# Optimization experiments

Hardware: AMD Instinct MI355X
Metric: run time of the kernel (lower is better)

The kernel has to match this reference:

```python
import jax, jax.numpy as jnp
import numpy as np

K = 10  # kNN neighbors (module default)


def _safe_norm(x):
    # norm along last axis with zero (not NaN) gradient at x == 0
    sq = jnp.sum(x * x, axis=-1)
    safe = jnp.where(sq > 0, sq, 1.0)
    return jnp.where(sq > 0, jnp.sqrt(safe), 0.0)


def _angle(v1, v2):
    cross = jnp.cross(v1, v2, axis=-1)
    dot = jnp.sum(v1 * v2, axis=-1)
    return jnp.arctan2(_safe_norm(cross), dot)


def _compute_normals(p, k):
    # squared pairwise distances (same kNN ordering as cdist, cheaper/safer)
    sq = jnp.sum((p[:, None, :] - p[None, :, :]) ** 2, axis=-1)  # (N,N)
    _, knn = jax.lax.top_k(-sq, k + 1)
    knn = knn[:, 1:]                        # drop self, (N,k)
    neigh = p[knn]                          # (N,k,3)
    centered = neigh - neigh.mean(axis=1, keepdims=True)
    cov = jnp.einsum('nki,nkj->nij', centered, centered) / k  # (N,3,3)
    _, eigvecs = jnp.linalg.eigh(cov)
    return eigvecs[:, :, 0]                 # smallest-eigenvalue eigenvector, (N,3)


def reference(points, W, b):
    p = points[0]                           # (N,3)
    n = _compute_normals(p, K)              # (N,3)
    d = p[:, None, :] - p[None, :, :]       # (N,N,3), d[i,j] = p_i - p_j
    ni = jnp.broadcast_to(n[:, None, :], d.shape)
    nj = jnp.broadcast_to(n[None, :, :], d.shape)
    ppf = jnp.stack([
        _safe_norm(d),
        _angle(ni, d),
        _angle(nj, d),
        _angle(ni, nj),
    ], axis=-1)                             # (N,N,4)
    feat = ppf.mean(axis=1)                 # (N,4)
    s = feat @ W.T + b                      # (N,out)
    return s[None]                          # (1,N,out)


def setup_inputs() -> dict:
    key = jax.random.key(0)
    k1, k2 = jax.random.split(key)
    N, OUT = 2048, 256
    points = jax.random.normal(k1, (1, N, 3), dtype=jnp.float32)
    W = jax.random.normal(k2, (OUT, 4), dtype=jnp.float32) * 0.1
    b = jnp.zeros((OUT,), dtype=jnp.float32)
    return {"points": points, "W": W, "b": b}
```

## Files before the change

kernel.cpp:

```cpp
#include <hip/hip_runtime.h>
#include <math.h>

#pragma clang fp contract(off)

#define NPTS 2048
#define KNN 10
#define NOUT 256


__device__ __forceinline__ float lapy2f(float x, float y) {
  float xa = fabsf(x), ya = fabsf(y);
  float w = fmaxf(xa, ya), z = fminf(xa, ya);
  if (z == 0.f) return w;
  float t = z / w;
  return w * sqrtf(1.f + t * t);
}

__device__ __forceinline__ void slartgf(float f, float g, float& c, float& s, float& r) {
  if (g == 0.f) { c = 1.f; s = 0.f; r = f; }
  else if (f == 0.f) { c = 0.f; s = copysignf(1.f, g); r = fabsf(g); }
  else {
    float d = sqrtf(f * f + g * g);
    float p = 1.f / d;
    c = fabsf(f) * p;
    s = g * copysignf(p, f);
    r = copysignf(d, f);
  }
}

__device__ __forceinline__ void slaev2f(float a, float b, float c,
                                        float& rt1, float& rt2, float& cs1, float& sn1) {
  float sm = a + c;
  float df = a - c;
  float adf = fabsf(df);
  float tb = b + b;
  float ab = fabsf(tb);
  float acmx, acmn;
  if (fabsf(a) > fabsf(c)) { acmx = a; acmn = c; } else { acmx = c; acmn = a; }
  float rt;
  if (adf > ab)      { float t = ab / adf; rt = adf * sqrtf(1.f + t * t); }
  else if (adf < ab) { float t = adf / ab; rt = ab * sqrtf(1.f + t * t); }
  else               { rt = ab * sqrtf(2.f); }
  int sgn1;
  if (sm < 0.f) {
    rt1 = 0.5f * (sm - rt); sgn1 = -1;
    rt2 = (acmx / rt1) * acmn - (b / rt1) * b;
  } else if (sm > 0.f) {
    rt1 = 0.5f * (sm + rt); sgn1 = 1;
    rt2 = (acmx / rt1) * acmn - (b / rt1) * b;
  } else {
    rt1 = 0.5f * rt; rt2 = -0.5f * rt; sgn1 = 1;
  }
  int sgn2; float cs;
  if (df >= 0.f) { cs = df + rt; sgn2 = 1; } else { cs = df - rt; sgn2 = -1; }
  float acs = fabsf(cs);
  if (acs > ab) {
    float ct = -tb / cs;
    sn1 = 1.f / sqrtf(1.f + ct * ct);
    cs1 = ct * sn1;
  } else {
    if (ab == 0.f) { cs1 = 1.f; sn1 = 0.f; }
    else {
      float tn = -cs / tb;
      cs1 = 1.f / sqrtf(1.f + tn * tn);
      sn1 = tn * cs1;
    }
  }
  if (sgn1 == sgn2) { float tn = cs1; cs1 = -sn1; sn1 = tn; }
}

#define ROT12(c, s) {                                         \
    float t_;                                                 \
    t_ = z01; z01 = (c) * t_ - (s) * z00; z00 = (s) * t_ + (c) * z00; \
    t_ = z11; z11 = (c) * t_ - (s) * z10; z10 = (s) * t_ + (c) * z10; \
    t_ = z21; z21 = (c) * t_ - (s) * z20; z20 = (s) * t_ + (c) * z20; }
#define ROT23(c, s) {                                         \
    float t_;                                                 \
    t_ = z02; z02 = (c) * t_ - (s) * z01; z01 = (s) * t_ + (c) * z01; \
    t_ = z12; z12 = (c) * t_ - (s) * z11; z11 = (s) * t_ + (c) * z11; \
    t_ = z22; z22 = (c) * t_ - (s) * z21; z21 = (s) * t_ + (c) * z21; }

__device__ __forceinline__ void ssteqr3_reg(
    float& d0, float& d1, float& d2, float& e0, float& e1,
    float& z00, float& z01, float& z02,
    float& z10, float& z11, float& z12,
    float& z20, float& z21, float& z22) {
  const float eps = 5.9604645e-8f;
  const float eps2 = eps * eps;
  const float safmin = 1.1754944e-38f;
  const int nmaxit = 90;
  int jtot = 0;
  int l1 = 1;
  for (int og = 0; og < 4; ++og) {
    if (l1 > 3) break;
    if (l1 == 2) e0 = 0.f;
    else if (l1 == 3) e1 = 0.f;
    int m = 3;
    if (l1 == 1) {
      float t = fabsf(e0);
      if (t == 0.f) m = 1;
      else if (t <= (sqrtf(fabsf(d0)) * sqrtf(fabsf(d1))) * eps) { e0 = 0.f; m = 1; }
      else {
        float t2 = fabsf(e1);
        if (t2 == 0.f) m = 2;
        else if (t2 <= (sqrtf(fabsf(d1)) * sqrtf(fabsf(d2))) * eps) { e1 = 0.f; m = 2; }
      }
    } else if (l1 == 2) {
      float t = fabsf(e1);
      if (t == 0.f) m = 2;
      else if (t <= (sqrtf(fabsf(d1)) * sqrtf(fabsf(d2))) * eps) { e1 = 0.f; m = 2; }
    }
    int l = l1, lend = m;
    l1 = m + 1;
    if (lend == l) continue;
    {
      float dlend = (lend == 1) ? d0 : ((lend == 2) ? d1 : d2);
      float dl = (l == 1) ? d0 : ((l == 2) ? d1 : d2);
      if (fabsf(dlend) < fabsf(dl)) { int t = lend; lend = l; l = t; }
    }
    if (lend > l) {
      for (int it = 0; it < 128; ++it) {
        int m2 = lend;
        if (l != lend) {
          for (int mm = l; mm <= lend - 1; ++mm) {
            float em  = (mm == 1) ? e0 : e1;
            float dm1 = (mm == 1) ? d0 : d1;
            float dm  = (mm == 1) ? d1 : d2;
            float tst = em * em;
            if (tst <= (eps2 * fabsf(dm1)) * fabsf(dm) + safmin) { m2 = mm; break; }
          }
        }
        if (m2 < lend) { if (m2 == 1) e0 = 0.f; else e1 = 0.f; }
        float p = (l == 1) ? d0 : ((l == 2) ? d1 : d2);
        if (m2 == l) { l += 1; if (l <= lend) continue; break; }
        if (m2 == l + 1) {
          float rt1, rt2, c, s;
          if (l == 1) {
            slaev2f(d0, e0, d1, rt1, rt2, c, s);
            ROT12(c, s)
            d0 = rt1; d1 = rt2; e0 = 0.f;
          } else {
            slaev2f(d1, e1, d2, rt1, rt2, c, s);
            ROT23(c, s)
            d1 = rt1; d2 = rt2; e1 = 0.f;
          }
          l += 2; if (l <= lend) continue; break;
        }
        if (jtot == nmaxit) break;
        jtot++;
        float g = (d1 - p) / (2.f * e0);
        float r = lapy2f(g, 1.f);
        g = d2 - p + e0 / (g + copysignf(r, g));
        float s = 1.f, c = 1.f;
        p = 0.f;
        float c0, s0n, c1, s1n;
        {
          float f = s * e1;
          float bb = c * e1;
          slartgf(g, f, c, s, r);
          g = d2 - p;
          r = (d1 - g) * s + 2.f * c * bb;
          p = s * r;
          d2 = g + p;
          g = c * r - bb;
          c1 = c; s1n = -s;
        }
        {
          float f = s * e0;
          float bb = c * e0;
          slartgf(g, f, c, s, r);
          e1 = r;
          g = d1 - p;
          r = (d0 - g) * s + 2.f * c * bb;
          p = s * r;
          d1 = g + p;
          g = c * r - bb;
          c0 = c; s0n = -s;
        }
        ROT23(c1, s1n)
        ROT12(c0, s0n)
        d0 = d0 - p;
        e0 = g;
      }
    } else {
      for (int it = 0; it < 128; ++it) {
        int m2 = lend;
        if (l != lend) {
          for (int mm = l; mm >= lend + 1; --mm) {
            float em  = (mm == 3) ? e1 : e0;
            float dm1 = (mm == 3) ? d2 : d1;
            float dm2 = (mm == 3) ? d1 : d0;
            float tst = em * em;
            if (tst <= (eps2 * fabsf(dm1)) * fabsf(dm2) + safmin) { m2 = mm; break; }
          }
        }
        if (m2 > lend) { if (m2 == 3) e1 = 0.f; else e0 = 0.f; }
        float p = (l == 1) ? d0 : ((l == 2) ? d1 : d2);
        if (m2 == l) { l -= 1; if (l >= lend) continue; break; }
        if (m2 == l - 1) {
          float rt1, rt2, c, s;
          if (l == 2) {
            slaev2f(d0, e0, d1, rt1, rt2, c, s);
            ROT12(c, s)
            d0 = rt1; d1 = rt2; e0 = 0.f;
          } else {
            slaev2f(d1, e1, d2, rt1, rt2, c, s);
            ROT23(c, s)
            d1 = rt1; d2 = rt2; e1 = 0.f;
          }
          l -= 2; if (l >= lend) continue; break;
        }
        if (jtot == nmaxit) break;
        jtot++;
        float g = (d1 - p) / (2.f * e1);
        float r = lapy2f(g, 1.f);
        g = d0 - p + e1 / (g + copysignf(r, g));
        float s = 1.f, c = 1.f;
        p = 0.f;
        float c0, s0p, c1, s1p;
        {
          float f = s * e0;
          float bb = c * e0;
          slartgf(g, f, c, s, r);
          g = d0 - p;
          r = (d1 - g) * s + 2.f * c * bb;
          p = s * r;
          d0 = g + p;
          g = c * r - bb;
          c0 = c; s0p = s;
        }
        {
          float f = s * e1;
          float bb = c * e1;
          slartgf(g, f, c, s, r);
          e0 = r;
          g = d1 - p;
          r = (d2 - g) * s + 2.f * c * bb;
          p = s * r;
          d1 = g + p;
          g = c * r - bb;
          c1 = c; s1p = s;
        }
        ROT12(c0, s0p)
        ROT23(c1, s1p)
        d2 = d2 - p;
        e1 = g;
      }
    }
  }
  {
    int k = 1; float p = d0;
    if (d1 < p) { k = 2; p = d1; }
    if (d2 < p) { k = 3; p = d2; }
    if (k == 2) {
      d1 = d0; d0 = p;
      float t;
      t = z00; z00 = z01; z01 = t;
      t = z10; z10 = z11; z11 = t;
      t = z20; z20 = z21; z21 = t;
    } else if (k == 3) {
      d2 = d0; d0 = p;
      float t;
      t = z00; z00 = z02; z02 = t;
      t = z10; z10 = z12; z12 = t;
      t = z20; z20 = z22; z22 = t;
    }
    k = 2; p = d1;
    if (d2 < p) { k = 3; p = d2; }
    if (k == 3) {
      d2 = d1; d1 = p;
      float t;
      t = z01; z01 = z02; z02 = t;
      t = z11; z11 = z12; z12 = t;
      t = z21; z21 = z22; z22 = t;
    }
  }
}


__global__ __launch_bounds__(256) void knn_normals_kernel(
    const float* __restrict__ pts,
    float* __restrict__ pxa, float* __restrict__ pya, float* __restrict__ pza,
    float* __restrict__ nxa, float* __restrict__ nya, float* __restrict__ nza) {
  __shared__ int knn_lds[4][KNN];
  const int tid = threadIdx.x;
  const int lane = tid & 63;
  const int wv = tid >> 6;

  {
    const int p = 4 * blockIdx.x + wv;
    float px = pts[3 * p], py = pts[3 * p + 1], pz = pts[3 * p + 2];
    if (lane == 0) { pxa[p] = px; pya[p] = py; pza[p] = pz; }

    unsigned long long k0[8], k1[8], k2[8], k3[8];
#define DIST(g, arr)                                                      \
    {                                                                     \
      _Pragma("unroll")                                                   \
      for (int t = 0; t < 8; ++t) {                                       \
        int j = ((g) * 8 + t) * 64 + lane;                                \
        float dx = px - pts[3 * j];                                       \
        float dy = py - pts[3 * j + 1];                                   \
        float dz = pz - pts[3 * j + 2];                                   \
        float sq = dx * dx;                                               \
        sq = sq + dy * dy;                                                \
        sq = sq + dz * dz;                                                \
        arr[t] = (((unsigned long long)__float_as_uint(sq)) << 32) |      \
                 (unsigned int)j;                                         \
      }                                                                   \
    }
    DIST(0, k0) DIST(1, k1) DIST(2, k2) DIST(3, k3)
#undef DIST

#define CE(arr, a, b)                                                     \
    {                                                                     \
      unsigned long long lo = arr[a] < arr[b] ? arr[a] : arr[b];          \
      unsigned long long hi = arr[a] < arr[b] ? arr[b] : arr[a];          \
      arr[a] = lo; arr[b] = hi;                                           \
    }
#define SORT8(arr)                                                        \
    CE(arr, 0, 1) CE(arr, 2, 3) CE(arr, 4, 5) CE(arr, 6, 7)               \
    CE(arr, 0, 2) CE(arr, 1, 3) CE(arr, 4, 6) CE(arr, 5, 7)               \
    CE(arr, 1, 2) CE(arr, 5, 6) CE(arr, 0, 4) CE(arr, 3, 7)               \
    CE(arr, 1, 5) CE(arr, 2, 6)                                           \
    CE(arr, 1, 4) CE(arr, 3, 6)                                           \
    CE(arr, 2, 4) CE(arr, 3, 5)                                           \
    CE(arr, 3, 4)
    SORT8(k0) SORT8(k1) SORT8(k2) SORT8(k3)
#undef SORT8
#undef CE

#define POP(arr)                                                          \
    {                                                                     \
      _Pragma("unroll")                                                   \
      for (int q = 0; q < 7; ++q) arr[q] = arr[q + 1];                    \
      arr[7] = 0xFFFFFFFFFFFFFFFFULL;                                     \
    }
    for (int r = 0; r < KNN + 1; ++r) {
      unsigned long long h01 = k0[0] < k1[0] ? k0[0] : k1[0];
      unsigned long long h23 = k2[0] < k3[0] ? k2[0] : k3[0];
      unsigned long long h = h01 < h23 ? h01 : h23;
      unsigned long long m = h;
#pragma unroll
      for (int off = 32; off > 0; off >>= 1) {
        unsigned long long o = __shfl_xor(m, off, 64);
        m = (o < m) ? o : m;
      }
      if (r > 0 && lane == 0) knn_lds[wv][r - 1] = (int)(unsigned int)m;
      if (h == m) {
        if (k0[0] == m)      { POP(k0) }
        else if (k1[0] == m) { POP(k1) }
        else if (k2[0] == m) { POP(k2) }
        else                 { POP(k3) }
      }
    }
#undef POP
  }
  __syncthreads();

  if (tid < 4) {
    const int p = 4 * blockIdx.x + tid;
    float nx[KNN], ny[KNN], nz[KNN];
    float sx = 0.f, sy = 0.f, sz = 0.f;
#pragma unroll
    for (int t = 0; t < KNN; ++t) {
      int j = knn_lds[tid][t];
      nx[t] = pts[3 * j]; ny[t] = pts[3 * j + 1]; nz[t] = pts[3 * j + 2];
      sx = sx + nx[t]; sy = sy + ny[t]; sz = sz + nz[t];
    }
    float mx = sx / 10.f, my = sy / 10.f, mz = sz / 10.f;
    float a11 = 0.f, a21 = 0.f, a31 = 0.f, a22 = 0.f, a32 = 0.f, a33 = 0.f;
#pragma unroll
    for (int t = 0; t < KNN; ++t) {
      float cx = nx[t] - mx, cy = ny[t] - my, cz = nz[t] - mz;
      a11 = a11 + cx * cx;
      a21 = a21 + cy * cx;
      a31 = a31 + cz * cx;
      a22 = a22 + cy * cy;
      a32 = a32 + cz * cy;
      a33 = a33 + cz * cz;
    }
    a11 = a11 / 10.f; a21 = a21 / 10.f; a31 = a31 / 10.f;
    a22 = a22 / 10.f; a32 = a32 / 10.f; a33 = a33 / 10.f;

    float d0, d1, d2, e0, e1, tau1 = 0.f, v2 = 0.f;
    {
      float alpha = a21;
      float xnorm = fabsf(a31);
      if (xnorm == 0.f) {
        tau1 = 0.f; v2 = 0.f;
        d0 = a11; d1 = a22; d2 = a33; e0 = alpha; e1 = a32;
      } else {
        float beta = -copysignf(lapy2f(alpha, xnorm), alpha);
        tau1 = (beta - alpha) / beta;
        v2 = a31 * (1.f / (alpha - beta));
        float y1 = tau1 * a22; y1 = y1 + tau1 * (a32 * v2);
        float y2 = tau1 * a32; y2 = y2 + (tau1 * v2) * a33;
        float dotv = y1; dotv = dotv + y2 * v2;
        float ac = -0.5f * tau1 * dotv;
        y1 = y1 + ac;
        y2 = y2 + ac * v2;
        float t1 = -y1, t2 = -1.f;
        a22 = (a22 + t1) + y1 * t2;
        a32 = (a32 + v2 * t1) + y2 * t2;
        float t1b = -y2, t2b = -v2;
        a33 = (a33 + v2 * t1b) + y2 * t2b;
        d0 = a11; d1 = a22; d2 = a33; e0 = beta; e1 = a32;
      }
    }
    float z00 = 1.f, z01 = 0.f, z02 = 0.f;
    float z10 = 0.f, z11 = 1.f, z12 = 0.f;
    float z20 = 0.f, z21 = 0.f, z22 = 1.f;
    ssteqr3_reg(d0, d1, d2, e0, e1,
                z00, z01, z02, z10, z11, z12, z20, z21, z22);
    if (tau1 != 0.f) {
      float w = tau1 * (z10 + v2 * z20);
      z10 = z10 - w;
      z20 = z20 - v2 * w;
    }
    nxa[p] = z00;
    nya[p] = z10;
    nza[p] = z20;
  }
}


__device__ __forceinline__ float atan2_pos(float y, float x) {
#pragma clang fp contract(fast)
  float axx = fabsf(x);
  float mn = fminf(axx, y), mx = fmaxf(axx, y);
  float a = mn * __builtin_amdgcn_rcpf(mx);
  a = (mx == 0.f) ? 0.f : a;
  float s = a * a;
  float r = a * (0.9998660f +
           s * (-0.3302995f +
           s * (0.1801410f +
           s * (-0.0851330f +
           s * 0.0208351f))));
  r = (y > axx) ? 1.57079632679f - r : r;
  r = (x < 0.f) ? 3.14159265359f - r : r;
  return r;
}

__device__ __forceinline__ float angle3(float ax, float ay, float az,
                                        float bx, float by, float bz) {
#pragma clang fp contract(fast)
  float cx = ay * bz - az * by;
  float cy = az * bx - ax * bz;
  float cz = ax * by - ay * bx;
  float sq = cx * cx + cy * cy + cz * cz;
  float dot = ax * bx + ay * by + az * bz;
  return atan2_pos(sqrtf(sq), dot);
}

__global__ __launch_bounds__(256) void ppf_kernel(
    const float* __restrict__ pxa, const float* __restrict__ pya,
    const float* __restrict__ pza, const float* __restrict__ nxa,
    const float* __restrict__ nya, const float* __restrict__ nza,
    const float* __restrict__ Wm, const float* __restrict__ bias,
    float* __restrict__ out) {
#pragma clang fp contract(fast)
  const int tid = threadIdx.x;
  const int lane = tid & 63;
  const int wv = tid >> 6;
  const int i = 4 * blockIdx.x + wv;

  float pxi = pxa[i], pyi = pya[i], pzi = pza[i];
  float ax = nxa[i], ay = nya[i], az = nza[i];

  float s0 = 0.f, s1 = 0.f, s2 = 0.f, s3 = 0.f;
#pragma unroll 4
  for (int it = 0; it < NPTS / 64; ++it) {
    int j = it * 64 + lane;
    float dx = pxi - pxa[j];
    float dy = pyi - pya[j];
    float dz = pzi - pza[j];
    float bx = nxa[j], by = nya[j], bz = nza[j];
    float sq = dx * dx + dy * dy + dz * dz;
    s0 += sqrtf(sq);
    s1 += angle3(ax, ay, az, dx, dy, dz);
    s2 += angle3(bx, by, bz, dx, dy, dz);
    s3 += angle3(ax, ay, az, bx, by, bz);
  }

#pragma unroll
  for (int off = 1; off < 64; off <<= 1) {
    s0 += __shfl_xor(s0, off, 64);
    s1 += __shfl_xor(s1, off, 64);
    s2 += __shfl_xor(s2, off, 64);
    s3 += __shfl_xor(s3, off, 64);
  }
  const float inv = 1.f / 2048.f;
  float f0 = s0 * inv, f1 = s1 * inv, f2 = s2 * inv, f3 = s3 * inv;

  const float4* W4 = (const float4*)Wm;
  const float4* b4 = (const float4*)bias;
  float4 bb = b4[lane];
  float4 w0 = W4[4 * lane + 0];
  float4 w1 = W4[4 * lane + 1];
  float4 w2 = W4[4 * lane + 2];
  float4 w3 = W4[4 * lane + 3];
  float4 r;
  r.x = (((f0 * w0.x + f1 * w0.y) + f2 * w0.z) + f3 * w0.w) + bb.x;
  r.y = (((f0 * w1.x + f1 * w1.y) + f2 * w1.z) + f3 * w1.w) + bb.y;
  r.z = (((f0 * w2.x + f1 * w2.y) + f2 * w2.z) + f3 * w2.w) + bb.z;
  r.w = (((f0 * w3.x + f1 * w3.y) + f2 * w3.z) + f3 * w3.w) + bb.w;
  ((float4*)(out + (size_t)i * NOUT))[lane] = r;
}


extern "C" void kernel_launch(void* const* d_in, const int* in_sizes, int n_in,
                              void* d_out, int out_size, void* d_ws, size_t ws_size,
                              hipStream_t stream) {
  const float* pts = (const float*)d_in[0];
  const float* Wm  = (const float*)d_in[1];
  const float* bs  = (const float*)d_in[2];
  float* out = (float*)d_out;

  float* pxa = (float*)d_ws;
  float* pya = pxa + NPTS;
  float* pza = pya + NPTS;
  float* nxa = pza + NPTS;
  float* nya = nxa + NPTS;
  float* nza = nya + NPTS;

  knn_normals_kernel<<<NPTS / 4, 256, 0, stream>>>(pts, pxa, pya, pza, nxa, nya, nza);
  ppf_kernel<<<NPTS / 4, 256, 0, stream>>>(pxa, pya, pza, nxa, nya, nza, Wm, bs, out);
}
```

Before: 110.3 us.

## Split each point across four wavefronts in kNN and PPF kernels

Both kernels now give one point to a whole 256-thread block instead of one point per wavefront. Each wave handles a quarter of the candidates and combines its partial top-11 or partial sums through shared memory; the kNN merge ranks the 44 candidates. The aim is four times more blocks, more parallelism across the GPU and shorter serial loops per wave. In exchange it adds block synchronisation and a single-thread normal computation in every block. It also switches sqrt to the raw AMDGPU builtin.

Measured after the change: 99.44 us. -9.9%, faster.

```diff
diff --git a/kernel.cpp b/kernel.cpp
--- a/kernel.cpp
+++ b/kernel.cpp
@@ -282,88 +282,79 @@
     const float* __restrict__ pts,
     float* __restrict__ pxa, float* __restrict__ pya, float* __restrict__ pza,
     float* __restrict__ nxa, float* __restrict__ nya, float* __restrict__ nza) {
-  __shared__ int knn_lds[4][KNN];
+  __shared__ unsigned long long cand[4 * (KNN + 1)];
+  __shared__ int knn_sh[KNN];
   const int tid = threadIdx.x;
   const int lane = tid & 63;
   const int wv = tid >> 6;
+  const int p = blockIdx.x;
 
   {
-    const int p = 4 * blockIdx.x + wv;
     float px = pts[3 * p], py = pts[3 * p + 1], pz = pts[3 * p + 2];
-    if (lane == 0) { pxa[p] = px; pya[p] = py; pza[p] = pz; }
-
-    unsigned long long k0[8], k1[8], k2[8], k3[8];
-#define DIST(g, arr)                                                      \
+    if (tid == 0) { pxa[p] = px; pya[p] = py; pza[p] = pz; }
+
+    unsigned long long k0[8];
+#pragma unroll
+    for (int t = 0; t < 8; ++t) {
+      int j = wv * 512 + t * 64 + lane;
+      float dx = px - pts[3 * j];
+      float dy = py - pts[3 * j + 1];
+      float dz = pz - pts[3 * j + 2];
+      float sq = dx * dx;
+      sq = sq + dy * dy;
+      sq = sq + dz * dz;
+      k0[t] = (((unsigned long long)__float_as_uint(sq)) << 32) |
+              (unsigned int)j;
+    }
+
+#define CE(a, b)                                                          \
     {                                                                     \
-      _Pragma("unroll")                                                   \
-      for (int t = 0; t < 8; ++t) {                                       \
-        int j = ((g) * 8 + t) * 64 + lane;                                \
-        float dx = px - pts[3 * j];                                       \
-        float dy = py - pts[3 * j + 1];                                   \
-        float dz = pz - pts[3 * j + 2];                                   \
-        float sq = dx * dx;                                               \
-        sq = sq + dy * dy;                                                \
-        sq = sq + dz * dz;                                                \
-        arr[t] = (((unsigned long long)__float_as_uint(sq)) << 32) |      \
-                 (unsigned int)j;                                         \
-      }                                                                   \
-    }
-    DIST(0, k0) DIST(1, k1) DIST(2, k2) DIST(3, k3)
-#undef DIST
-
-#define CE(arr, a, b)                                                     \
-    {                                                                     \
-      unsigned long long lo = arr[a] < arr[b] ? arr[a] : arr[b];          \
-      unsigned long long hi = arr[a] < arr[b] ? arr[b] : arr[a];          \
-      arr[a] = lo; arr[b] = hi;                                           \
-    }
-#define SORT8(arr)                                                        \
-    CE(arr, 0, 1) CE(arr, 2, 3) CE(arr, 4, 5) CE(arr, 6, 7)               \
-    CE(arr, 0, 2) CE(arr, 1, 3) CE(arr, 4, 6) CE(arr, 5, 7)               \
-    CE(arr, 1, 2) CE(arr, 5, 6) CE(arr, 0, 4) CE(arr, 3, 7)               \
-    CE(arr, 1, 5) CE(arr, 2, 6)                                           \
-    CE(arr, 1, 4) CE(arr, 3, 6)                                           \
-    CE(arr, 2, 4) CE(arr, 3, 5)                                           \
-    CE(arr, 3, 4)
-    SORT8(k0) SORT8(k1) SORT8(k2) SORT8(k3)
-#undef SORT8
+      unsigned long long lo = k0[a] < k0[b] ? k0[a] : k0[b];              \
+      unsigned long long hi = k0[a] < k0[b] ? k0[b] : k0[a];              \
+      k0[a] = lo; k0[b] = hi;                                             \
+    }
+    CE(0, 1) CE(2, 3) CE(4, 5) CE(6, 7)
+    CE(0, 2) CE(1, 3) CE(4, 6) CE(5, 7)
+    CE(1, 2) CE(5, 6) CE(0, 4) CE(3, 7)
+    CE(1, 5) CE(2, 6)
+    CE(1, 4) CE(3, 6)
+    CE(2, 4) CE(3, 5)
+    CE(3, 4)
 #undef CE
 
-#define POP(arr)                                                          \
-    {                                                                     \
-      _Pragma("unroll")                                                   \
-      for (int q = 0; q < 7; ++q) arr[q] = arr[q + 1];                    \
-      arr[7] = 0xFFFFFFFFFFFFFFFFULL;                                     \
-    }
     for (int r = 0; r < KNN + 1; ++r) {
-      unsigned long long h01 = k0[0] < k1[0] ? k0[0] : k1[0];
-      unsigned long long h23 = k2[0] < k3[0] ? k2[0] : k3[0];
-      unsigned long long h = h01 < h23 ? h01 : h23;
-      unsigned long long m = h;
+      unsigned long long m = k0[0];
 #pragma unroll
       for (int off = 32; off > 0; off >>= 1) {
         unsigned long long o = __shfl_xor(m, off, 64);
         m = (o < m) ? o : m;
       }
-      if (r > 0 && lane == 0) knn_lds[wv][r - 1] = (int)(unsigned int)m;
-      if (h == m) {
-        if (k0[0] == m)      { POP(k0) }
-        else if (k1[0] == m) { POP(k1) }
-        else if (k2[0] == m) { POP(k2) }
-        else                 { POP(k3) }
+      if (lane == 0) cand[wv * (KNN + 1) + r] = m;
+      if (k0[0] == m) {
+#pragma unroll
+        for (int q = 0; q < 7; ++q) k0[q] = k0[q + 1];
+        k0[7] = 0xFFFFFFFFFFFFFFFFULL;
       }
     }
-#undef POP
   }
   __syncthreads();
 
-  if (tid < 4) {
-    const int p = 4 * blockIdx.x + tid;
+  if (tid < 4 * (KNN + 1)) {
+    unsigned long long e = cand[tid];
+    int rank = 0;
+#pragma unroll
+    for (int m = 0; m < 4 * (KNN + 1); ++m) rank += (cand[m] < e) ? 1 : 0;
+    if (rank > 0 && rank <= KNN)
+      knn_sh[rank - 1] = (int)(unsigned int)(e & 0xFFFFFFFFULL);
+  }
+  __syncthreads();
+
+  if (tid == 0) {
     float nx[KNN], ny[KNN], nz[KNN];
     float sx = 0.f, sy = 0.f, sz = 0.f;
 #pragma unroll
     for (int t = 0; t < KNN; ++t) {
-      int j = knn_lds[tid][t];
+      int j = knn_sh[t];
       nx[t] = pts[3 * j]; ny[t] = pts[3 * j + 1]; nz[t] = pts[3 * j + 2];
       sx = sx + nx[t]; sy = sy + ny[t]; sz = sz + nz[t];
     }
@@ -449,7 +440,7 @@
   float cz = ax * by - ay * bx;
   float sq = cx * cx + cy * cy + cz * cz;
   float dot = ax * bx + ay * by + az * bz;
-  return atan2_pos(sqrtf(sq), dot);
+  return atan2_pos(__builtin_amdgcn_sqrtf(sq), dot);
 }
 
 __global__ __launch_bounds__(256) void ppf_kernel(
@@ -459,24 +450,25 @@
     const float* __restrict__ Wm, const float* __restrict__ bias,
     float* __restrict__ out) {
 #pragma clang fp contract(fast)
+  __shared__ float ps[4][4];
   const int tid = threadIdx.x;
   const int lane = tid & 63;
   const int wv = tid >> 6;
-  const int i = 4 * blockIdx.x + wv;
+  const int i = blockIdx.x;
 
   float pxi = pxa[i], pyi = pya[i], pzi = pza[i];
   float ax = nxa[i], ay = nya[i], az = nza[i];
 
   float s0 = 0.f, s1 = 0.f, s2 = 0.f, s3 = 0.f;
-#pragma unroll 4
-  for (int it = 0; it < NPTS / 64; ++it) {
-    int j = it * 64 + lane;
+#pragma unroll
+  for (int it = 0; it < 8; ++it) {
+    int j = wv * 512 + it * 64 + lane;
     float dx = pxi - pxa[j];
     float dy = pyi - pya[j];
     float dz = pzi - pza[j];
     float bx = nxa[j], by = nya[j], bz = nza[j];
     float sq = dx * dx + dy * dy + dz * dz;
-    s0 += sqrtf(sq);
+    s0 += __builtin_amdgcn_sqrtf(sq);
     s1 += angle3(ax, ay, az, dx, dy, dz);
     s2 += angle3(bx, by, bz, dx, dy, dz);
     s3 += angle3(ax, ay, az, bx, by, bz);
@@ -489,22 +481,18 @@
     s2 += __shfl_xor(s2, off, 64);
     s3 += __shfl_xor(s3, off, 64);
   }
+  if (lane == 0) { ps[wv][0] = s0; ps[wv][1] = s1; ps[wv][2] = s2; ps[wv][3] = s3; }
+  __syncthreads();
+
   const float inv = 1.f / 2048.f;
-  float f0 = s0 * inv, f1 = s1 * inv, f2 = s2 * inv, f3 = s3 * inv;
-
-  const float4* W4 = (const float4*)Wm;
-  const float4* b4 = (const float4*)bias;
-  float4 bb = b4[lane];
-  float4 w0 = W4[4 * lane + 0];
-  float4 w1 = W4[4 * lane + 1];
-  float4 w2 = W4[4 * lane + 2];
-  float4 w3 = W4[4 * lane + 3];
-  float4 r;
-  r.x = (((f0 * w0.x + f1 * w0.y) + f2 * w0.z) + f3 * w0.w) + bb.x;
-  r.y = (((f0 * w1.x + f1 * w1.y) + f2 * w1.z) + f3 * w1.w) + bb.y;
-  r.z = (((f0 * w2.x + f1 * w2.y) + f2 * w2.z) + f3 * w2.w) + bb.z;
-  r.w = (((f0 * w3.x + f1 * w3.y) + f2 * w3.z) + f3 * w3.w) + bb.w;
-  ((float4*)(out + (size_t)i * NOUT))[lane] = r;
+  float f0 = ((ps[0][0] + ps[1][0]) + (ps[2][0] + ps[3][0])) * inv;
+  float f1 = ((ps[0][1] + ps[1][1]) + (ps[2][1] + ps[3][1])) * inv;
+  float f2 = ((ps[0][2] + ps[1][2]) + (ps[2][2] + ps[3][2])) * inv;
+  float f3 = ((ps[0][3] + ps[1][3]) + (ps[2][3] + ps[3][3])) * inv;
+
+  float4 w = ((const float4*)Wm)[tid];
+  float r = (((f0 * w.x + f1 * w.y) + f2 * w.z) + f3 * w.w) + bias[tid];
+  out[(size_t)i * NOUT + tid] = r;
 }
 
 
@@ -523,6 +511,6 @@
   float* nya = nxa + NPTS;
   float* nza = nya + NPTS;
 
-  knn_normals_kernel<<<NPTS / 4, 256, 0, stream>>>(pts, pxa, pya, pza, nxa, nya, nza);
-  ppf_kernel<<<NPTS / 4, 256, 0, stream>>>(pxa, pya, pza, nxa, nya, nza, Wm, bs, out);
-}
+  knn_normals_kernel<<<NPTS, 256, 0, stream>>>(pts, pxa, pya, pza, nxa, nya, nza);
+  ppf_kernel<<<NPTS, 256, 0, stream>>>(pxa, pya, pza, nxa, nya, nza, Wm, bs, out);
+}
```
